# Kernel tuning notes

Hardware: AMD Instinct MI355X
Metric: run time of the kernel (lower is better)

## Reference

```python
import math
import jax, jax.numpy as jnp
import numpy as np

B, D, C = 2, 1024, 512          # (b*f with f=1), spatial tokens, channels
H, DH = 8, 64                   # heads, head dim (H*DH == C)
P = 32                          # past length == temporal_max_len
MAX_LEN = 32
HID = max(128, C // 2)          # refiner hidden

def make_pe():
    # sinusoidal APE buffer, shape [MAX_LEN, C]
    position = np.arange(MAX_LEN)[:, None].astype(np.float32)
    div_term = np.exp(np.arange(0, C, 2).astype(np.float32) * (-math.log(10000.0) / C))
    pe = np.zeros((MAX_LEN, C), dtype=np.float32)
    pe[:, 0::2] = np.sin(position * div_term)
    pe[:, 1::2] = np.cos(position * div_term)
    return jnp.asarray(pe)

def setup_inputs() -> dict:
    key = jax.random.key(0)
    ks = jax.random.split(key, 12)
    sc = 0.02
    return {
        "hidden_states": jax.random.normal(ks[0], (B, D, C), jnp.float32),
        "cached_hidden_states": jax.random.normal(ks[1], (B * D, P, C), jnp.float32),
        "Wq": jax.random.normal(ks[2], (C, C), jnp.float32) * sc,
        "Wk": jax.random.normal(ks[3], (C, C), jnp.float32) * sc,
        "Wv": jax.random.normal(ks[4], (C, C), jnp.float32) * sc,
        "Wo": jax.random.normal(ks[5], (C, C), jnp.float32) * sc,
        "bo": jnp.zeros((C,), jnp.float32),
        "W1": jax.random.normal(ks[6], (3 * C, HID), jnp.float32) * sc,
        "b1": jnp.zeros((HID,), jnp.float32),
        "W2": jax.random.normal(ks[7], (HID, 2 * C + 2), jnp.float32) * sc,
        "b2": jnp.zeros((2 * C + 2,), jnp.float32),
        "pe": make_pe(),
        "select_top_r": 8,
    }

def reference(hidden_states, cached_hidden_states, Wq, Wk, Wv, Wo, bo, W1, b1, W2, b2, pe, select_top_r):
    b, d, c = hidden_states.shape
    B0 = b * d
    # '(b f) d c -> (b d) f c' with f=1
    now = hidden_states.reshape(B0, 1, c)
    past = cached_hidden_states                      # [B0, P, C]
    # APE positional encoding
    now_pos = now + pe[:1][None]
    past_pos = past + pe[: past.shape[1]][None]
    # projections (no bias, diffusers CrossAttention style)
    q_now = now_pos @ Wq                             # [B0, 1, C]
    k_now = now_pos @ Wk
    v_now = now_pos @ Wv
    k_past = past_pos @ Wk                           # [B0, P, C]
    v_past = past_pos @ Wv
    # top-r key selection over past
    score = jnp.einsum('bqc,bpc->bqp', q_now, k_past)[:, 0]   # [B0, P]
    _, idx = jax.lax.top_k(score, select_top_r)               # [B0, R]
    k_sel = jnp.take_along_axis(k_past, idx[:, :, None], axis=1)  # [B0, R, C]
    v_sel = jnp.take_along_axis(v_past, idx[:, :, None], axis=1)
    # refiner MLP: concat(q, k, v) -> hidden -> 2C+2
    R = k_sel.shape[1]
    q_rep = jnp.broadcast_to(q_now, (B0, R, c))
    inp = jnp.concatenate([q_rep, k_sel, v_sel], axis=-1)     # [B0, R, 3C]
    h = jax.nn.gelu(inp @ W1 + b1, approximate=False)
    out = h @ W2 + b2                                         # [B0, R, 2C+2]
    dK, dV, log_s, logit_g = jnp.split(out, [c, 2 * c, 2 * c + 1], axis=-1)
    s = jax.nn.softplus(log_s) + 1e-5
    g = jax.nn.sigmoid(logit_g)
    k_sel = k_sel + g * dK * s
    v_sel = v_sel + g * dV * s
    # attention over [selected past ; now]
    key_ = jnp.concatenate([k_sel, k_now], axis=1)            # [B0, R+1, C]
    val_ = jnp.concatenate([v_sel, v_now], axis=1)
    L = key_.shape[1]
    qh = q_now.reshape(B0, 1, H, DH)
    kh = key_.reshape(B0, L, H, DH)
    vh = val_.reshape(B0, L, H, DH)
    scale = DH ** -0.5
    logits = jnp.einsum('bqhd,bkhd->bhqk', qh, kh) * scale
    attn = jax.nn.softmax(logits, axis=-1)
    ctx = jnp.einsum('bhqk,bkhd->bqhd', attn, vh).reshape(B0, 1, c)
    out_proj = ctx @ Wo + bo                                  # [B0, 1, C]
    # '(b d) f c -> (b f) d c' with f=1
    return out_proj.reshape(b, d, c)
```

## Files before the change

### kernel.cpp

```cpp
#include <hip/hip_runtime.h>
#include <math.h>


typedef __attribute__((ext_vector_type(8))) __bf16 bf16x8;
typedef __attribute__((ext_vector_type(4))) float f32x4;
typedef unsigned short u16;
typedef unsigned int u32;

static __device__ __forceinline__ float4 ld4(const float* p) { return *(const float4*)p; }
static __device__ __forceinline__ float gelu_exact(float x) {
  return 0.5f * x * (1.0f + erff(x * 0.70710678118654752f));
}
static __device__ __forceinline__ u16 f2bf(float f) {
  u32 u = __float_as_uint(f);
  u = (u + 0x7fffu + ((u >> 16) & 1u)) >> 16;
  return (u16)u;
}
static __device__ __forceinline__ float bf2f(u16 h) {
  return __uint_as_float(((u32)h) << 16);
}
static __device__ __forceinline__ u32 pk2(float a, float b) {
  return (u32)f2bf(a) | ((u32)f2bf(b) << 16);
}
static __device__ __forceinline__ void ld8bf(const u16* p, float* o) {
  int4 v = *(const int4*)p;
  o[0] = bf2f((u16)((u32)v.x & 0xffffu)); o[1] = bf2f((u16)(((u32)v.x) >> 16));
  o[2] = bf2f((u16)((u32)v.y & 0xffffu)); o[3] = bf2f((u16)(((u32)v.y) >> 16));
  o[4] = bf2f((u16)((u32)v.z & 0xffffu)); o[5] = bf2f((u16)(((u32)v.z) >> 16));
  o[6] = bf2f((u16)((u32)v.w & 0xffffu)); o[7] = bf2f((u16)(((u32)v.w) >> 16));
}
static __device__ __forceinline__ void gld16(const void* g, void* l) {
  __builtin_amdgcn_global_load_lds((const __attribute__((address_space(1))) void*)g,
                                   (__attribute__((address_space(3))) void*)l, 16, 0, 0);
}

__global__ __launch_bounds__(256) void prep_all(
    const float* __restrict__ Wq, const float* __restrict__ Wk,
    const float* __restrict__ Wv, const float* __restrict__ W1,
    const float* __restrict__ W2, const float* __restrict__ Wo,
    u16* __restrict__ Wqkvt, u16* __restrict__ W1t,
    u16* __restrict__ W2t, u16* __restrict__ Wot,
    float* __restrict__ Wqk) {
  const int b = blockIdx.x;
  if (b < 1664) {
    __shared__ float t[32][33];
    const float* S; u16* D; int lds_, Kd, nx, t0;
    if (b < 256)       { S = Wq; D = Wqkvt;              lds_ = 512;  Kd = 512;  nx = 16; t0 = 0; }
    else if (b < 512)  { S = Wk; D = Wqkvt + 512 * 512;  lds_ = 512;  Kd = 512;  nx = 16; t0 = 256; }
    else if (b < 768)  { S = Wv; D = Wqkvt + 1024 * 512; lds_ = 512;  Kd = 512;  nx = 16; t0 = 512; }
    else if (b < 1152) { S = W1; D = W1t;                lds_ = 256;  Kd = 1536; nx = 8;  t0 = 768; }
    else if (b < 1408) { S = W2; D = W2t;                lds_ = 1026; Kd = 256;  nx = 32; t0 = 1152; }
    else               { S = Wo; D = Wot;                lds_ = 512;  Kd = 512;  nx = 16; t0 = 1408; }
    const int tile = b - t0;
    const int n0 = (tile % nx) << 5, k0 = (tile / nx) << 5;
    const int tx = threadIdx.x & 31, ty8 = threadIdx.x >> 5;
    for (int yy = ty8; yy < 32; yy += 8)
      t[yy][tx] = S[(size_t)(k0 + yy) * lds_ + n0 + tx];
    __syncthreads();
    for (int yy = ty8; yy < 32; yy += 8)
      D[(size_t)(n0 + yy) * Kd + k0 + tx] = f2bf(t[tx][yy]);
  } else {
    __shared__ float Aq[32][36];
    __shared__ float Bk[32][36];
    const int tile = b - 1664;
    const int c0 = (tile >> 4) << 5, j0 = (tile & 15) << 5;
    const int tid = threadIdx.x;
    const int r = tid >> 3, ic = (tid & 7) << 2;
    const int ty = tid >> 4, tx = tid & 15;
    float a00 = 0.f, a01 = 0.f, a10 = 0.f, a11 = 0.f;
    for (int i0 = 0; i0 < 512; i0 += 32) {
      float4 a = ld4(Wq + (size_t)(c0 + r) * 512 + i0 + ic);
      float4 bb = ld4(Wk + (size_t)(j0 + r) * 512 + i0 + ic);
      Aq[r][ic] = a.x; Aq[r][ic + 1] = a.y; Aq[r][ic + 2] = a.z; Aq[r][ic + 3] = a.w;
      Bk[r][ic] = bb.x; Bk[r][ic + 1] = bb.y; Bk[r][ic + 2] = bb.z; Bk[r][ic + 3] = bb.w;
      __syncthreads();
#pragma unroll
      for (int i = 0; i < 32; ++i) {
        float x0 = Aq[ty * 2][i], x1 = Aq[ty * 2 + 1][i];
        float y0 = Bk[tx * 2][i], y1 = Bk[tx * 2 + 1][i];
        a00 += x0 * y0; a01 += x0 * y1; a10 += x1 * y0; a11 += x1 * y1;
      }
      __syncthreads();
    }
    Wqk[(size_t)(c0 + ty * 2) * 512 + j0 + tx * 2]         = a00;
    Wqk[(size_t)(c0 + ty * 2) * 512 + j0 + tx * 2 + 1]     = a01;
    Wqk[(size_t)(c0 + ty * 2 + 1) * 512 + j0 + tx * 2]     = a10;
    Wqk[(size_t)(c0 + ty * 2 + 1) * 512 + j0 + tx * 2 + 1] = a11;
  }
}

__global__ __launch_bounds__(256) void qk_gemm(const float* __restrict__ A,
                                               const float* __restrict__ B,
                                               float* __restrict__ C,
                                               const float* __restrict__ pe) {
  __shared__ float As[16][68];
  __shared__ float Bs[16][68];
  const int tid = threadIdx.x;
  const int rm = blockIdx.y << 6, cn = blockIdx.x << 6;
  const int tx = tid & 15, ty = tid >> 4;
  const int ar = tid >> 2, ak = (tid & 3) << 2;
  const int bk = tid >> 4, bn = (tid & 15) << 2;
  const float* Ap = A + (size_t)(rm + ar) * 512;
  float acc[4][4] = {};
  for (int kt = 0; kt < 32; ++kt) {
    const int k0 = (kt << 4) + ak;
    float4 x = ld4(Ap + k0);
    float4 p4 = ld4(pe + k0);
    As[ak + 0][ar] = x.x + p4.x; As[ak + 1][ar] = x.y + p4.y;
    As[ak + 2][ar] = x.z + p4.z; As[ak + 3][ar] = x.w + p4.w;
    *(float4*)&Bs[bk][bn] = ld4(B + (size_t)((kt << 4) + bk) * 512 + cn + bn);
    __syncthreads();
#pragma unroll
    for (int kk = 0; kk < 16; ++kk) {
      float4 a = *(const float4*)&As[kk][ty << 2];
      float4 b = *(const float4*)&Bs[kk][tx << 2];
      acc[0][0] += a.x * b.x; acc[0][1] += a.x * b.y; acc[0][2] += a.x * b.z; acc[0][3] += a.x * b.w;
      acc[1][0] += a.y * b.x; acc[1][1] += a.y * b.y; acc[1][2] += a.y * b.z; acc[1][3] += a.y * b.w;
      acc[2][0] += a.z * b.x; acc[2][1] += a.z * b.y; acc[2][2] += a.z * b.z; acc[2][3] += a.z * b.w;
      acc[3][0] += a.w * b.x; acc[3][1] += a.w * b.y; acc[3][2] += a.w * b.z; acc[3][3] += a.w * b.w;
    }
    __syncthreads();
  }
  const int row0 = rm + (ty << 2), col0 = cn + (tx << 2);
#pragma unroll
  for (int i = 0; i < 4; ++i)
    *(float4*)(C + (size_t)(row0 + i) * 512 + col0) =
        make_float4(acc[i][0], acc[i][1], acc[i][2], acc[i][3]);
}

__global__ __launch_bounds__(256) void score_topk_gather(
    const float* __restrict__ QK, const float* __restrict__ cached,
    const float* __restrict__ pe, const float* __restrict__ hidden,
    u16* __restrict__ xh, u16* __restrict__ gsel) {
  __shared__ float sc[32];
  __shared__ int ix[8];
  const int b0 = blockIdx.x;
  const int tid = threadIdx.x;
  const int w = tid >> 6, lane = tid & 63;
  const int off = lane << 3;
  const float* qk = QK + (size_t)b0 * 512;
  float4 q0 = ld4(qk + off);
  float4 q1 = ld4(qk + off + 4);
  for (int i = 0; i < 8; ++i) {
    const int p = (w << 3) + i;
    const float* cp = cached + ((size_t)b0 * 32 + p) * 512 + off;
    const float* pp = pe + (size_t)p * 512 + off;
    float4 c0 = ld4(cp), c1 = ld4(cp + 4);
    float4 e0 = ld4(pp), e1 = ld4(pp + 4);
    float s = (c0.x + e0.x) * q0.x + (c0.y + e0.y) * q0.y +
              (c0.z + e0.z) * q0.z + (c0.w + e0.w) * q0.w +
              (c1.x + e1.x) * q1.x + (c1.y + e1.y) * q1.y +
              (c1.z + e1.z) * q1.z + (c1.w + e1.w) * q1.w;
#pragma unroll
    for (int d = 32; d > 0; d >>= 1) s += __shfl_xor(s, d);
    if (lane == 0) sc[p] = s;
  }
  __syncthreads();
  if (tid == 0) {
    for (int r = 0; r < 8; ++r) {
      float best = -INFINITY; int bi = 0;
      for (int p = 0; p < 32; ++p) {
        float v = sc[p];
        if (v > best) { best = v; bi = p; }
      }
      ix[r] = bi;
      sc[bi] = -INFINITY;
    }
  }
  __syncthreads();
#pragma unroll
  for (int rr = 0; rr < 2; ++rr) {
    const int rsel = w + (rr << 2);
    const int p = ix[rsel];
    const float* cp = cached + ((size_t)b0 * 32 + p) * 512 + off;
    const float* pp = pe + (size_t)p * 512 + off;
    float4 c0 = ld4(cp), c1 = ld4(cp + 4);
    float4 e0 = ld4(pp), e1 = ld4(pp + 4);
    int4 o;
    o.x = pk2(c0.x + e0.x, c0.y + e0.y);
    o.y = pk2(c0.z + e0.z, c0.w + e0.w);
    o.z = pk2(c1.x + e1.x, c1.y + e1.y);
    o.w = pk2(c1.z + e1.z, c1.w + e1.w);
    *(int4*)(gsel + (size_t)(b0 * 8 + rsel) * 512 + off) = o;
  }
  if (w == 0) {
    const float* hp = hidden + (size_t)b0 * 512 + off;
    float4 a = ld4(hp), b = ld4(hp + 4);
    float4 p0 = ld4(pe + off), p1 = ld4(pe + off + 4);
    int4 o;
    o.x = pk2(a.x + p0.x, a.y + p0.y);
    o.y = pk2(a.z + p0.z, a.w + p0.w);
    o.z = pk2(b.x + p1.x, b.y + p1.y);
    o.w = pk2(b.z + p1.z, b.w + p1.w);
    *(int4*)(xh + (size_t)b0 * 512 + off) = o;
  }
}

__global__ __launch_bounds__(256) void bgemm_fused1(
    const u16* __restrict__ gsel, const u16* __restrict__ xh,
    const u16* __restrict__ Wqkvt, u16* __restrict__ kvh,
    u16* __restrict__ Yh) {
  __shared__ u16 As[4096];
  __shared__ u16 Bs[4096];
  const int tid = threadIdx.x, lane = tid & 63, w = tid >> 6;
  const int bid = blockIdx.x;
  const int srow = tid >> 2, skoff = (tid & 3) << 3;
  const u16 *a0, *b0; u16* C; int ldc, rm, cn;
  if (bid < 1024) {
    rm = (bid >> 3) << 7; cn = (bid & 7) << 7;
    a0 = gsel + (size_t)(rm + srow) * 512 + skoff;
    b0 = Wqkvt + (size_t)(512 + cn + srow) * 512 + skoff;
    C = kvh; ldc = 1024;
  } else {
    const int b2 = bid - 1024;
    rm = (b2 / 12) << 7; cn = (b2 % 12) << 7;
    a0 = xh + (size_t)(rm + srow) * 512 + skoff;
    b0 = Wqkvt + (size_t)(cn + srow) * 512 + skoff;
    C = Yh; ldc = 1536;
  }
  const u16* a1 = a0 + (size_t)64 * 512;
  const u16* b1 = b0 + (size_t)64 * 512;
  u16* aD0 = As + (w << 9); u16* aD1 = As + 2048 + (w << 9);
  u16* bD0 = Bs + (w << 9); u16* bD1 = Bs + 2048 + (w << 9);
  const int arb = ((((w >> 1) << 6) + (lane & 15)) << 5) + ((lane >> 4) << 3);
  const int brb = ((((w & 1) << 6) + (lane & 15)) << 5) + ((lane >> 4) << 3);
  f32x4 acc[4][4];
#pragma unroll
  for (int i = 0; i < 4; ++i)
#pragma unroll
    for (int j = 0; j < 4; ++j) acc[i][j] = (f32x4){0.f, 0.f, 0.f, 0.f};
  for (int kt = 0; kt < 16; ++kt) {
    const int ko = kt << 5;
    if (kt) __syncthreads();
    gld16(a0 + ko, aD0); gld16(a1 + ko, aD1);
    gld16(b0 + ko, bD0); gld16(b1 + ko, bD1);
    __syncthreads();
    bf16x8 av[4], bv[4];
#pragma unroll
    for (int i = 0; i < 4; ++i) av[i] = *(const bf16x8*)(As + arb + (i << 9));
#pragma unroll
    for (int j = 0; j < 4; ++j) bv[j] = *(const bf16x8*)(Bs + brb + (j << 9));
#pragma unroll
    for (int i = 0; i < 4; ++i)
#pragma unroll
      for (int j = 0; j < 4; ++j)
        acc[i][j] = __builtin_amdgcn_mfma_f32_16x16x32_bf16(av[i], bv[j], acc[i][j], 0, 0, 0);
  }
  const int row0 = rm + ((w >> 1) << 6) + ((lane >> 4) << 2);
  const int col0 = cn + ((w & 1) << 6) + (lane & 15);
#pragma unroll
  for (int j = 0; j < 4; ++j) {
    const int col = col0 + (j << 4);
#pragma unroll
    for (int i = 0; i < 4; ++i)
#pragma unroll
      for (int r = 0; r < 4; ++r)
        C[(size_t)(row0 + (i << 4) + r) * ldc + col] = f2bf(acc[i][j][r]);
  }
}

__global__ __launch_bounds__(256) void mlp1_sg(
    const u16* __restrict__ Yh, const u16* __restrict__ kvh,
    const u16* __restrict__ W1t, const float* __restrict__ b1,
    const float* __restrict__ W2, const float* __restrict__ b2,
    u16* __restrict__ hb, float* __restrict__ sgv) {
  __shared__ u16 As[2048];
  __shared__ u16 Bs[8192];
  __shared__ float wa[256], wb[256];
  const int tid = threadIdx.x, lane = tid & 63, w = tid >> 6;
  const int rm = blockIdx.x << 6;
  const int srow = tid >> 2, skoff = (tid & 3) << 3;
  wa[tid] = W2[(size_t)tid * 1026 + 1024];
  wb[tid] = W2[(size_t)tid * 1026 + 1025];
  const int m0 = rm + srow;
  const u16* aq = Yh + (size_t)(m0 >> 3) * 1536 + skoff;
  const u16* akv = kvh + (size_t)m0 * 1024 + skoff;
  const u16* bsrc = W1t + (size_t)srow * 1536 + skoff;
  u16* aD = As + (w << 9);
  u16* bD0 = Bs + (w << 9);
  u16* bD1 = Bs + 2048 + (w << 9);
  u16* bD2 = Bs + 4096 + (w << 9);
  u16* bD3 = Bs + 6144 + (w << 9);
  const int arb = ((lane & 15) << 5) + ((lane >> 4) << 3);
  const int brb = (((w << 6) + (lane & 15)) << 5) + ((lane >> 4) << 3);
  f32x4 acc[4][4];
#pragma unroll
  for (int i = 0; i < 4; ++i)
#pragma unroll
    for (int j = 0; j < 4; ++j) acc[i][j] = (f32x4){0.f, 0.f, 0.f, 0.f};
  for (int kt = 0; kt < 48; ++kt) {
    const int ko = kt << 5;
    if (kt) __syncthreads();
    if (kt < 16) gld16(aq + ko, aD);
    else         gld16(akv + ko - 512, aD);
    gld16(bsrc + ko, bD0);
    gld16(bsrc + (size_t)64 * 1536 + ko, bD1);
    gld16(bsrc + (size_t)128 * 1536 + ko, bD2);
    gld16(bsrc + (size_t)192 * 1536 + ko, bD3);
    __syncthreads();
    bf16x8 av[4], bv[4];
#pragma unroll
    for (int i = 0; i < 4; ++i) av[i] = *(const bf16x8*)(As + arb + (i << 9));
#pragma unroll
    for (int j = 0; j < 4; ++j) bv[j] = *(const bf16x8*)(Bs + brb + (j << 9));
#pragma unroll
    for (int i = 0; i < 4; ++i)
#pragma unroll
      for (int j = 0; j < 4; ++j)
        acc[i][j] = __builtin_amdgcn_mfma_f32_16x16x32_bf16(av[i], bv[j], acc[i][j], 0, 0, 0);
  }
  const int row0 = rm + ((lane >> 4) << 2);
  const int col0 = (w << 6) + (lane & 15);
#pragma unroll
  for (int j = 0; j < 4; ++j) {
    const int col = col0 + (j << 4);
    const float bc = b1[col];
#pragma unroll
    for (int i = 0; i < 4; ++i)
#pragma unroll
      for (int r = 0; r < 4; ++r)
        hb[(size_t)(row0 + (i << 4) + r) * 256 + col] = f2bf(gelu_exact(acc[i][j][r] + bc));
  }
  __syncthreads();
  const int row = tid >> 2, q = tid & 3;
  const int rr = rm + row;
  const u16* hp = hb + (size_t)rr * 256 + (q << 6);
  float pa = 0.f, pb = 0.f;
  for (int c = 0; c < 64; c += 8) {
    float h[8]; ld8bf(hp + c, h);
    const int cb = (q << 6) + c;
#pragma unroll
    for (int t = 0; t < 8; ++t) { pa += h[t] * wa[cb + t]; pb += h[t] * wb[cb + t]; }
  }
  pa += __shfl_xor(pa, 1); pa += __shfl_xor(pa, 2);
  pb += __shfl_xor(pb, 1); pb += __shfl_xor(pb, 2);
  if (q == 0) {
    const float t0 = pa + b2[1024];
    const float t1 = pb + b2[1025];
    const float s = (t0 > 0.f ? t0 + log1pf(expf(-t0)) : log1pf(expf(t0))) + 1e-5f;
    const float g = 1.f / (1.f + expf(-t1));
    sgv[2 * rr] = s; sgv[2 * rr + 1] = g;
  }
}

__global__ __launch_bounds__(256) void bgemm_delta(
    const u16* __restrict__ hb, const u16* __restrict__ W2t,
    u16* __restrict__ kvh, const float* __restrict__ b2,
    const float* __restrict__ sgv) {
  __shared__ u16 As[4096];
  __shared__ u16 Bs[4096];
  const int tid = threadIdx.x, lane = tid & 63, w = tid >> 6;
  const int rm = blockIdx.y << 7, cn = blockIdx.x << 7;
  const int srow = tid >> 2, skoff = (tid & 3) << 3;
  const u16* a0 = hb + (size_t)(rm + srow) * 256 + skoff;
  const u16* a1 = a0 + (size_t)64 * 256;
  const u16* b0 = W2t + (size_t)(cn + srow) * 256 + skoff;
  const u16* b1 = b0 + (size_t)64 * 256;
  u16* aD0 = As + (w << 9); u16* aD1 = As + 2048 + (w << 9);
  u16* bD0 = Bs + (w << 9); u16* bD1 = Bs + 2048 + (w << 9);
  const int arb = ((((w >> 1) << 6) + (lane & 15)) << 5) + ((lane >> 4) << 3);
  const int brb = ((((w & 1) << 6) + (lane & 15)) << 5) + ((lane >> 4) << 3);
  f32x4 acc[4][4];
#pragma unroll
  for (int i = 0; i < 4; ++i)
#pragma unroll
    for (int j = 0; j < 4; ++j) acc[i][j] = (f32x4){0.f, 0.f, 0.f, 0.f};
  for (int kt = 0; kt < 8; ++kt) {
    const int ko = kt << 5;
    if (kt) __syncthreads();
    gld16(a0 + ko, aD0); gld16(a1 + ko, aD1);
    gld16(b0 + ko, bD0); gld16(b1 + ko, bD1);
    __syncthreads();
    bf16x8 av[4], bv[4];
#pragma unroll
    for (int i = 0; i < 4; ++i) av[i] = *(const bf16x8*)(As + arb + (i << 9));
#pragma unroll
    for (int j = 0; j < 4; ++j) bv[j] = *(const bf16x8*)(Bs + brb + (j << 9));
#pragma unroll
    for (int i = 0; i < 4; ++i)
#pragma unroll
      for (int j = 0; j < 4; ++j)
        acc[i][j] = __builtin_amdgcn_mfma_f32_16x16x32_bf16(av[i], bv[j], acc[i][j], 0, 0, 0);
  }
  const int row0 = rm + ((w >> 1) << 6) + ((lane >> 4) << 2);
  const int col0 = cn + ((w & 1) << 6) + (lane & 15);
  float bc[4];
#pragma unroll
  for (int j = 0; j < 4; ++j) bc[j] = b2[col0 + (j << 4)];
#pragma unroll
  for (int i = 0; i < 4; ++i)
#pragma unroll
    for (int r = 0; r < 4; ++r) {
      const int rr = row0 + (i << 4) + r;
      const float gs = sgv[2 * rr] * sgv[2 * rr + 1];
      u16* p = kvh + (size_t)rr * 1024 + col0;
#pragma unroll
      for (int j = 0; j < 4; ++j) {
        const int o = j << 4;
        p[o] = f2bf(bf2f(p[o]) + gs * (acc[i][j][r] + bc[j]));
      }
    }
}

__global__ __launch_bounds__(256) void attn2(const u16* __restrict__ Yh,
                                             const u16* __restrict__ kvh,
                                             u16* __restrict__ ctxh) {
  const int w = threadIdx.x >> 6, lane = threadIdx.x & 63;
  const int b0 = (blockIdx.x << 2) + w;
  const int off = lane << 3;
  const u16* yr = Yh + (size_t)b0 * 1536;
  float qv[8]; ld8bf(yr + off, qv);
  float lg[9];
#pragma unroll
  for (int k = 0; k < 9; ++k) {
    const u16* kr = (k < 8) ? (kvh + (size_t)(b0 * 8 + k) * 1024 + off)
                            : (yr + 512 + off);
    float kv[8]; ld8bf(kr, kv);
    float s = qv[0] * kv[0] + qv[1] * kv[1] + qv[2] * kv[2] + qv[3] * kv[3] +
              qv[4] * kv[4] + qv[5] * kv[5] + qv[6] * kv[6] + qv[7] * kv[7];
    s += __shfl_xor(s, 1); s += __shfl_xor(s, 2); s += __shfl_xor(s, 4);
    lg[k] = s * 0.125f;
  }
  float m = lg[0];
#pragma unroll
  for (int k = 1; k < 9; ++k) m = fmaxf(m, lg[k]);
  float sum = 0.f;
#pragma unroll
  for (int k = 0; k < 9; ++k) { lg[k] = expf(lg[k] - m); sum += lg[k]; }
  const float inv = 1.f / sum;
  float c[8] = {0.f, 0.f, 0.f, 0.f, 0.f, 0.f, 0.f, 0.f};
#pragma unroll
  for (int k = 0; k < 9; ++k) {
    const u16* vr = (k < 8) ? (kvh + (size_t)(b0 * 8 + k) * 1024 + 512 + off)
                            : (yr + 1024 + off);
    float vv[8]; ld8bf(vr, vv);
    const float wk = lg[k] * inv;
#pragma unroll
    for (int t = 0; t < 8; ++t) c[t] += wk * vv[t];
  }
  int4 o;
  o.x = pk2(c[0], c[1]); o.y = pk2(c[2], c[3]);
  o.z = pk2(c[4], c[5]); o.w = pk2(c[6], c[7]);
  *(int4*)(ctxh + (size_t)b0 * 512 + off) = o;
}

__global__ __launch_bounds__(256) void bgemm_out(
    const u16* __restrict__ ctxh, const u16* __restrict__ Wot,
    float* __restrict__ out, const float* __restrict__ bo) {
  __shared__ u16 As[4096];
  __shared__ u16 Bs[4096];
  const int tid = threadIdx.x, lane = tid & 63, w = tid >> 6;
  const int rm = blockIdx.y << 7, cn = blockIdx.x << 7;
  const int srow = tid >> 2, skoff = (tid & 3) << 3;
  const u16* a0 = ctxh + (size_t)(rm + srow) * 512 + skoff;
  const u16* a1 = a0 + (size_t)64 * 512;
  const u16* b0 = Wot + (size_t)(cn + srow) * 512 + skoff;
  const u16* b1 = b0 + (size_t)64 * 512;
  u16* aD0 = As + (w << 9); u16* aD1 = As + 2048 + (w << 9);
  u16* bD0 = Bs + (w << 9); u16* bD1 = Bs + 2048 + (w << 9);
  const int arb = ((((w >> 1) << 6) + (lane & 15)) << 5) + ((lane >> 4) << 3);
  const int brb = ((((w & 1) << 6) + (lane & 15)) << 5) + ((lane >> 4) << 3);
  f32x4 acc[4][4];
#pragma unroll
  for (int i = 0; i < 4; ++i)
#pragma unroll
    for (int j = 0; j < 4; ++j) acc[i][j] = (f32x4){0.f, 0.f, 0.f, 0.f};
  for (int kt = 0; kt < 16; ++kt) {
    const int ko = kt << 5;
    if (kt) __syncthreads();
    gld16(a0 + ko, aD0); gld16(a1 + ko, aD1);
    gld16(b0 + ko, bD0); gld16(b1 + ko, bD1);
    __syncthreads();
    bf16x8 av[4], bv[4];
#pragma unroll
    for (int i = 0; i < 4; ++i) av[i] = *(const bf16x8*)(As + arb + (i << 9));
#pragma unroll
    for (int j = 0; j < 4; ++j) bv[j] = *(const bf16x8*)(Bs + brb + (j << 9));
#pragma unroll
    for (int i = 0; i < 4; ++i)
#pragma unroll
      for (int j = 0; j < 4; ++j)
        acc[i][j] = __builtin_amdgcn_mfma_f32_16x16x32_bf16(av[i], bv[j], acc[i][j], 0, 0, 0);
  }
  const int row0 = rm + ((w >> 1) << 6) + ((lane >> 4) << 2);
  const int col0 = cn + ((w & 1) << 6) + (lane & 15);
  float bc[4];
#pragma unroll
  for (int j = 0; j < 4; ++j) bc[j] = bo[col0 + (j << 4)];
#pragma unroll
  for (int j = 0; j < 4; ++j)
#pragma unroll
    for (int i = 0; i < 4; ++i)
#pragma unroll
      for (int r = 0; r < 4; ++r)
        out[(size_t)(row0 + (i << 4) + r) * 512 + col0 + (j << 4)] = acc[i][j][r] + bc[j];
}

extern "C" void kernel_launch(void* const* d_in, const int* in_sizes, int n_in,
                              void* d_out, int out_size, void* d_ws, size_t ws_size,
                              hipStream_t stream) {
  const float* hidden = (const float*)d_in[0];
  const float* cached = (const float*)d_in[1];
  const float* Wq = (const float*)d_in[2];
  const float* Wk = (const float*)d_in[3];
  const float* Wv = (const float*)d_in[4];
  const float* Wo = (const float*)d_in[5];
  const float* bo = (const float*)d_in[6];
  const float* W1 = (const float*)d_in[7];
  const float* b1 = (const float*)d_in[8];
  const float* W2 = (const float*)d_in[9];
  const float* b2 = (const float*)d_in[10];
  const float* pe = (const float*)d_in[11];

  float* ws = (float*)d_ws;
  float* Wqk = ws;
  float* qkb = Wqk + 262144;
  float* sgv = qkb + 1048576;
  u16* Wqkvt = (u16*)(sgv + 32768);
  u16* W1t   = Wqkvt + 786432;
  u16* W2t   = W1t + 393216;
  u16* Wot   = W2t + 262144;
  u16* xh    = Wot + 262144;
  u16* gsel  = xh + 1048576;
  u16* Yh    = gsel + 8388608;
  u16* kvh   = Yh + 3145728;
  u16* hb    = kvh + 16777216;
  u16* ctxh  = hb + 4194304;
  float* out = (float*)d_out;
  (void)in_sizes; (void)n_in; (void)out_size; (void)ws_size;

  prep_all<<<dim3(1920), 256, 0, stream>>>(Wq, Wk, Wv, W1, W2, Wo,
                                           Wqkvt, W1t, W2t, Wot, Wqk);
  qk_gemm<<<dim3(8, 32), 256, 0, stream>>>(hidden, Wqk, qkb, pe);
  score_topk_gather<<<dim3(2048), 256, 0, stream>>>(qkb, cached, pe, hidden, xh, gsel);
  bgemm_fused1<<<dim3(1216), 256, 0, stream>>>(gsel, xh, Wqkvt, kvh, Yh);
  mlp1_sg<<<dim3(256), 256, 0, stream>>>(Yh, kvh, W1t, b1, W2, b2, hb, sgv);
  bgemm_delta<<<dim3(8, 128), 256, 0, stream>>>(hb, W2t, kvh, b2, sgv);
  attn2<<<dim3(512), 256, 0, stream>>>(Yh, kvh, ctxh);
  bgemm_out<<<dim3(4, 16), 256, 0, stream>>>(ctxh, Wot, out, bo);
}
```

Measured before the change: 443.0 us.

## Double K-tile depth in MFMA GEMMs and swap operands for vectorized epilogue stores

All four bf16 MFMA GEMM kernels now stage a 64-wide K slice per iteration instead of 32. That halves the loop trip count and the number of barrier pairs, at the cost of doubling LDS per block. The MFMA operands are swapped so each lane holds four consecutive output columns. This lets the epilogues write packed int2 bf16 or float4 fp32 values and read bias as float4, replacing the earlier scalar, strided stores. The larger LDS footprint may lower occupancy.

```diff
diff --git a/kernel.cpp b/kernel.cpp
--- a/kernel.cpp
+++ b/kernel.cpp
@@ -32,6 +32,14 @@
 static __device__ __forceinline__ void gld16(const void* g, void* l) {
   __builtin_amdgcn_global_load_lds((const __attribute__((address_space(1))) void*)g,
                                    (__attribute__((address_space(3))) void*)l, 16, 0, 0);
+}
+template <int NI>
+static __device__ __forceinline__ void stageT(u16* __restrict__ lds,
+                                              const u16* __restrict__ sp,
+                                              int ldk, int w) {
+#pragma unroll
+  for (int i = 0; i < NI; ++i)
+    gld16(sp + (size_t)(i << 5) * ldk, lds + (w << 9) + (i << 11));
 }
 
 __global__ __launch_bounds__(256) void prep_all(
@@ -200,62 +208,61 @@
     const u16* __restrict__ gsel, const u16* __restrict__ xh,
     const u16* __restrict__ Wqkvt, u16* __restrict__ kvh,
     u16* __restrict__ Yh) {
-  __shared__ u16 As[4096];
-  __shared__ u16 Bs[4096];
+  __shared__ u16 As[8192];
+  __shared__ u16 Bs[8192];
   const int tid = threadIdx.x, lane = tid & 63, w = tid >> 6;
   const int bid = blockIdx.x;
-  const int srow = tid >> 2, skoff = (tid & 3) << 3;
-  const u16 *a0, *b0; u16* C; int ldc, rm, cn;
+  int rm, cn, ldc; const u16 *Ab, *Bb; u16* C;
   if (bid < 1024) {
     rm = (bid >> 3) << 7; cn = (bid & 7) << 7;
-    a0 = gsel + (size_t)(rm + srow) * 512 + skoff;
-    b0 = Wqkvt + (size_t)(512 + cn + srow) * 512 + skoff;
-    C = kvh; ldc = 1024;
+    Ab = gsel; Bb = Wqkvt + (size_t)512 * 512; C = kvh; ldc = 1024;
   } else {
     const int b2 = bid - 1024;
     rm = (b2 / 12) << 7; cn = (b2 % 12) << 7;
-    a0 = xh + (size_t)(rm + srow) * 512 + skoff;
-    b0 = Wqkvt + (size_t)(cn + srow) * 512 + skoff;
-    C = Yh; ldc = 1536;
-  }
-  const u16* a1 = a0 + (size_t)64 * 512;
-  const u16* b1 = b0 + (size_t)64 * 512;
-  u16* aD0 = As + (w << 9); u16* aD1 = As + 2048 + (w << 9);
-  u16* bD0 = Bs + (w << 9); u16* bD1 = Bs + 2048 + (w << 9);
-  const int arb = ((((w >> 1) << 6) + (lane & 15)) << 5) + ((lane >> 4) << 3);
-  const int brb = ((((w & 1) << 6) + (lane & 15)) << 5) + ((lane >> 4) << 3);
+    Ab = xh; Bb = Wqkvt; C = Yh; ldc = 1536;
+  }
+  const int lrow = (w << 3) + (lane >> 3), lko = (lane & 7) << 3;
+  const u16* ap = Ab + (size_t)(rm + lrow) * 512 + lko;
+  const u16* bp = Bb + (size_t)(cn + lrow) * 512 + lko;
+  const int aoff = ((w >> 1) << 12) + ((lane & 15) << 6) + ((lane >> 4) << 3);
+  const int boff = ((w & 1) << 12) + ((lane & 15) << 6) + ((lane >> 4) << 3);
   f32x4 acc[4][4];
 #pragma unroll
   for (int i = 0; i < 4; ++i)
 #pragma unroll
     for (int j = 0; j < 4; ++j) acc[i][j] = (f32x4){0.f, 0.f, 0.f, 0.f};
-  for (int kt = 0; kt < 16; ++kt) {
-    const int ko = kt << 5;
+  for (int kt = 0; kt < 8; ++kt) {
     if (kt) __syncthreads();
-    gld16(a0 + ko, aD0); gld16(a1 + ko, aD1);
-    gld16(b0 + ko, bD0); gld16(b1 + ko, bD1);
-    __syncthreads();
-    bf16x8 av[4], bv[4];
-#pragma unroll
-    for (int i = 0; i < 4; ++i) av[i] = *(const bf16x8*)(As + arb + (i << 9));
-#pragma unroll
-    for (int j = 0; j < 4; ++j) bv[j] = *(const bf16x8*)(Bs + brb + (j << 9));
-#pragma unroll
-    for (int i = 0; i < 4; ++i)
-#pragma unroll
-      for (int j = 0; j < 4; ++j)
-        acc[i][j] = __builtin_amdgcn_mfma_f32_16x16x32_bf16(av[i], bv[j], acc[i][j], 0, 0, 0);
-  }
-  const int row0 = rm + ((w >> 1) << 6) + ((lane >> 4) << 2);
-  const int col0 = cn + ((w & 1) << 6) + (lane & 15);
-#pragma unroll
-  for (int j = 0; j < 4; ++j) {
-    const int col = col0 + (j << 4);
-#pragma unroll
-    for (int i = 0; i < 4; ++i)
-#pragma unroll
-      for (int r = 0; r < 4; ++r)
-        C[(size_t)(row0 + (i << 4) + r) * ldc + col] = f2bf(acc[i][j][r]);
+    stageT<4>(As, ap, 512, w);
+    stageT<4>(Bs, bp, 512, w);
+    ap += 64; bp += 64;
+    __syncthreads();
+#pragma unroll
+    for (int s = 0; s < 2; ++s) {
+      bf16x8 av[4], bv[4];
+#pragma unroll
+      for (int i = 0; i < 4; ++i) av[i] = *(const bf16x8*)(As + aoff + (i << 10) + (s << 5));
+#pragma unroll
+      for (int j = 0; j < 4; ++j) bv[j] = *(const bf16x8*)(Bs + boff + (j << 10) + (s << 5));
+#pragma unroll
+      for (int i = 0; i < 4; ++i)
+#pragma unroll
+        for (int j = 0; j < 4; ++j)
+          acc[i][j] = __builtin_amdgcn_mfma_f32_16x16x32_bf16(bv[j], av[i], acc[i][j], 0, 0, 0);
+    }
+  }
+  const int row0 = rm + ((w >> 1) << 6) + (lane & 15);
+  const int col0 = cn + ((w & 1) << 6) + ((lane >> 4) << 2);
+#pragma unroll
+  for (int i = 0; i < 4; ++i) {
+    u16* cp = C + (size_t)(row0 + (i << 4)) * ldc + col0;
+#pragma unroll
+    for (int j = 0; j < 4; ++j) {
+      int2 o;
+      o.x = (int)pk2(acc[i][j][0], acc[i][j][1]);
+      o.y = (int)pk2(acc[i][j][2], acc[i][j][3]);
+      *(int2*)(cp + (j << 4)) = o;
+    }
   }
 }
 
@@ -264,62 +271,66 @@
     const u16* __restrict__ W1t, const float* __restrict__ b1,
     const float* __restrict__ W2, const float* __restrict__ b2,
     u16* __restrict__ hb, float* __restrict__ sgv) {
-  __shared__ u16 As[2048];
-  __shared__ u16 Bs[8192];
+  __shared__ u16 As[4096];
+  __shared__ u16 Bs[16384];
   __shared__ float wa[256], wb[256];
   const int tid = threadIdx.x, lane = tid & 63, w = tid >> 6;
   const int rm = blockIdx.x << 6;
-  const int srow = tid >> 2, skoff = (tid & 3) << 3;
   wa[tid] = W2[(size_t)tid * 1026 + 1024];
   wb[tid] = W2[(size_t)tid * 1026 + 1025];
-  const int m0 = rm + srow;
-  const u16* aq = Yh + (size_t)(m0 >> 3) * 1536 + skoff;
-  const u16* akv = kvh + (size_t)m0 * 1024 + skoff;
-  const u16* bsrc = W1t + (size_t)srow * 1536 + skoff;
-  u16* aD = As + (w << 9);
-  u16* bD0 = Bs + (w << 9);
-  u16* bD1 = Bs + 2048 + (w << 9);
-  u16* bD2 = Bs + 4096 + (w << 9);
-  u16* bD3 = Bs + 6144 + (w << 9);
-  const int arb = ((lane & 15) << 5) + ((lane >> 4) << 3);
-  const int brb = (((w << 6) + (lane & 15)) << 5) + ((lane >> 4) << 3);
+  const int lrow = (w << 3) + (lane >> 3), lko = (lane & 7) << 3;
+  const u16* aq0  = Yh + (size_t)((rm + lrow) >> 3) * 1536 + lko;
+  const u16* aq1  = Yh + (size_t)((rm + lrow + 32) >> 3) * 1536 + lko;
+  const u16* akv0 = kvh + (size_t)(rm + lrow) * 1024 + lko;
+  const u16* akv1 = kvh + (size_t)(rm + lrow + 32) * 1024 + lko;
+  const u16* bp = W1t + (size_t)lrow * 1536 + lko;
+  const int aoff = ((lane & 15) << 6) + ((lane >> 4) << 3);
+  const int boff = (w << 12) + aoff;
   f32x4 acc[4][4];
 #pragma unroll
   for (int i = 0; i < 4; ++i)
 #pragma unroll
     for (int j = 0; j < 4; ++j) acc[i][j] = (f32x4){0.f, 0.f, 0.f, 0.f};
-  for (int kt = 0; kt < 48; ++kt) {
-    const int ko = kt << 5;
+  for (int kt = 0; kt < 24; ++kt) {
+    const int ko = kt << 6;
     if (kt) __syncthreads();
-    if (kt < 16) gld16(aq + ko, aD);
-    else         gld16(akv + ko - 512, aD);
-    gld16(bsrc + ko, bD0);
-    gld16(bsrc + (size_t)64 * 1536 + ko, bD1);
-    gld16(bsrc + (size_t)128 * 1536 + ko, bD2);
-    gld16(bsrc + (size_t)192 * 1536 + ko, bD3);
-    __syncthreads();
-    bf16x8 av[4], bv[4];
-#pragma unroll
-    for (int i = 0; i < 4; ++i) av[i] = *(const bf16x8*)(As + arb + (i << 9));
-#pragma unroll
-    for (int j = 0; j < 4; ++j) bv[j] = *(const bf16x8*)(Bs + brb + (j << 9));
-#pragma unroll
-    for (int i = 0; i < 4; ++i)
-#pragma unroll
-      for (int j = 0; j < 4; ++j)
-        acc[i][j] = __builtin_amdgcn_mfma_f32_16x16x32_bf16(av[i], bv[j], acc[i][j], 0, 0, 0);
-  }
-  const int row0 = rm + ((lane >> 4) << 2);
-  const int col0 = (w << 6) + (lane & 15);
-#pragma unroll
-  for (int j = 0; j < 4; ++j) {
-    const int col = col0 + (j << 4);
-    const float bc = b1[col];
-#pragma unroll
-    for (int i = 0; i < 4; ++i)
-#pragma unroll
-      for (int r = 0; r < 4; ++r)
-        hb[(size_t)(row0 + (i << 4) + r) * 256 + col] = f2bf(gelu_exact(acc[i][j][r] + bc));
+    if (kt < 8) {
+      gld16(aq0 + ko, As + (w << 9));
+      gld16(aq1 + ko, As + (w << 9) + 2048);
+    } else {
+      gld16(akv0 + ko - 512, As + (w << 9));
+      gld16(akv1 + ko - 512, As + (w << 9) + 2048);
+    }
+    stageT<8>(Bs, bp, 1536, w);
+    bp += 64;
+    __syncthreads();
+#pragma unroll
+    for (int s = 0; s < 2; ++s) {
+      bf16x8 av[4], bv[4];
+#pragma unroll
+      for (int i = 0; i < 4; ++i) av[i] = *(const bf16x8*)(As + aoff + (i << 10) + (s << 5));
+#pragma unroll
+      for (int j = 0; j < 4; ++j) bv[j] = *(const bf16x8*)(Bs + boff + (j << 10) + (s << 5));
+#pragma unroll
+      for (int i = 0; i < 4; ++i)
+#pragma unroll
+        for (int j = 0; j < 4; ++j)
+          acc[i][j] = __builtin_amdgcn_mfma_f32_16x16x32_bf16(bv[j], av[i], acc[i][j], 0, 0, 0);
+    }
+  }
+  const int row0 = rm + (lane & 15);
+  const int col0 = (w << 6) + ((lane >> 4) << 2);
+#pragma unroll
+  for (int i = 0; i < 4; ++i) {
+    u16* hp = hb + (size_t)(row0 + (i << 4)) * 256 + col0;
+#pragma unroll
+    for (int j = 0; j < 4; ++j) {
+      float4 bb = ld4(b1 + col0 + (j << 4));
+      int2 o;
+      o.x = (int)pk2(gelu_exact(acc[i][j][0] + bb.x), gelu_exact(acc[i][j][1] + bb.y));
+      o.y = (int)pk2(gelu_exact(acc[i][j][2] + bb.z), gelu_exact(acc[i][j][3] + bb.w));
+      *(int2*)(hp + (j << 4)) = o;
+    }
   }
   __syncthreads();
   const int row = tid >> 2, q = tid & 3;
@@ -347,59 +358,62 @@
     const u16* __restrict__ hb, const u16* __restrict__ W2t,
     u16* __restrict__ kvh, const float* __restrict__ b2,
     const float* __restrict__ sgv) {
-  __shared__ u16 As[4096];
-  __shared__ u16 Bs[4096];
+  __shared__ u16 As[8192];
+  __shared__ u16 Bs[8192];
   const int tid = threadIdx.x, lane = tid & 63, w = tid >> 6;
   const int rm = blockIdx.y << 7, cn = blockIdx.x << 7;
-  const int srow = tid >> 2, skoff = (tid & 3) << 3;
-  const u16* a0 = hb + (size_t)(rm + srow) * 256 + skoff;
-  const u16* a1 = a0 + (size_t)64 * 256;
-  const u16* b0 = W2t + (size_t)(cn + srow) * 256 + skoff;
-  const u16* b1 = b0 + (size_t)64 * 256;
-  u16* aD0 = As + (w << 9); u16* aD1 = As + 2048 + (w << 9);
-  u16* bD0 = Bs + (w << 9); u16* bD1 = Bs + 2048 + (w << 9);
-  const int arb = ((((w >> 1) << 6) + (lane & 15)) << 5) + ((lane >> 4) << 3);
-  const int brb = ((((w & 1) << 6) + (lane & 15)) << 5) + ((lane >> 4) << 3);
+  const int lrow = (w << 3) + (lane >> 3), lko = (lane & 7) << 3;
+  const u16* ap = hb + (size_t)(rm + lrow) * 256 + lko;
+  const u16* bp = W2t + (size_t)(cn + lrow) * 256 + lko;
+  const int aoff = ((w >> 1) << 12) + ((lane & 15) << 6) + ((lane >> 4) << 3);
+  const int boff = ((w & 1) << 12) + ((lane & 15) << 6) + ((lane >> 4) << 3);
   f32x4 acc[4][4];
 #pragma unroll
   for (int i = 0; i < 4; ++i)
 #pragma unroll
     for (int j = 0; j < 4; ++j) acc[i][j] = (f32x4){0.f, 0.f, 0.f, 0.f};
-  for (int kt = 0; kt < 8; ++kt) {
-    const int ko = kt << 5;
+  for (int kt = 0; kt < 4; ++kt) {
     if (kt) __syncthreads();
-    gld16(a0 + ko, aD0); gld16(a1 + ko, aD1);
-    gld16(b0 + ko, bD0); gld16(b1 + ko, bD1);
-    __syncthreads();
-    bf16x8 av[4], bv[4];
-#pragma unroll
-    for (int i = 0; i < 4; ++i) av[i] = *(const bf16x8*)(As + arb + (i << 9));
-#pragma unroll
-    for (int j = 0; j < 4; ++j) bv[j] = *(const bf16x8*)(Bs + brb + (j << 9));
-#pragma unroll
-    for (int i = 0; i < 4; ++i)
-#pragma unroll
-      for (int j = 0; j < 4; ++j)
-        acc[i][j] = __builtin_amdgcn_mfma_f32_16x16x32_bf16(av[i], bv[j], acc[i][j], 0, 0, 0);
-  }
-  const int row0 = rm + ((w >> 1) << 6) + ((lane >> 4) << 2);
-  const int col0 = cn + ((w & 1) << 6) + (lane & 15);
-  float bc[4];
-#pragma unroll
-  for (int j = 0; j < 4; ++j) bc[j] = b2[col0 + (j << 4)];
-#pragma unroll
-  for (int i = 0; i < 4; ++i)
-#pragma unroll
-    for (int r = 0; r < 4; ++r) {
-      const int rr = row0 + (i << 4) + r;
-      const float gs = sgv[2 * rr] * sgv[2 * rr + 1];
-      u16* p = kvh + (size_t)rr * 1024 + col0;
-#pragma unroll
-      for (int j = 0; j < 4; ++j) {
-        const int o = j << 4;
-        p[o] = f2bf(bf2f(p[o]) + gs * (acc[i][j][r] + bc[j]));
-      }
-    }
+    stageT<4>(As, ap, 256, w);
+    stageT<4>(Bs, bp, 256, w);
+    ap += 64; bp += 64;
+    __syncthreads();
+#pragma unroll
+    for (int s = 0; s < 2; ++s) {
+      bf16x8 av[4], bv[4];
+#pragma unroll
+      for (int i = 0; i < 4; ++i) av[i] = *(const bf16x8*)(As + aoff + (i << 10) + (s << 5));
+#pragma unroll
+      for (int j = 0; j < 4; ++j) bv[j] = *(const bf16x8*)(Bs + boff + (j << 10) + (s << 5));
+#pragma unroll
+      for (int i = 0; i < 4; ++i)
+#pragma unroll
+        for (int j = 0; j < 4; ++j)
+          acc[i][j] = __builtin_amdgcn_mfma_f32_16x16x32_bf16(bv[j], av[i], acc[i][j], 0, 0, 0);
+    }
+  }
+  const int row0 = rm + ((w >> 1) << 6) + (lane & 15);
+  const int col0 = cn + ((w & 1) << 6) + ((lane >> 4) << 2);
+#pragma unroll
+  for (int i = 0; i < 4; ++i) {
+    const int row = row0 + (i << 4);
+    const float2 sg2 = *(const float2*)(sgv + (row << 1));
+    const float gs = sg2.x * sg2.y;
+    u16* cp = kvh + (size_t)row * 1024 + col0;
+#pragma unroll
+    for (int j = 0; j < 4; ++j) {
+      float4 bb = ld4(b2 + col0 + (j << 4));
+      int2 old = *(const int2*)(cp + (j << 4));
+      const float o0 = bf2f((u16)((u32)old.x & 0xffffu)) + gs * (acc[i][j][0] + bb.x);
+      const float o1 = bf2f((u16)(((u32)old.x) >> 16)) + gs * (acc[i][j][1] + bb.y);
+      const float o2 = bf2f((u16)((u32)old.y & 0xffffu)) + gs * (acc[i][j][2] + bb.z);
+      const float o3 = bf2f((u16)(((u32)old.y) >> 16)) + gs * (acc[i][j][3] + bb.w);
+      int2 nv;
+      nv.x = (int)pk2(o0, o1);
+      nv.y = (int)pk2(o2, o3);
+      *(int2*)(cp + (j << 4)) = nv;
+    }
+  }
 }
 
 __global__ __launch_bounds__(256) void attn2(const u16* __restrict__ Yh,
@@ -447,53 +461,52 @@
 __global__ __launch_bounds__(256) void bgemm_out(
     const u16* __restrict__ ctxh, const u16* __restrict__ Wot,
     float* __restrict__ out, const float* __restrict__ bo) {
-  __shared__ u16 As[4096];
-  __shared__ u16 Bs[4096];
+  __shared__ u16 As[8192];
+  __shared__ u16 Bs[8192];
   const int tid = threadIdx.x, lane = tid & 63, w = tid >> 6;
   const int rm = blockIdx.y << 7, cn = blockIdx.x << 7;
-  const int srow = tid >> 2, skoff = (tid & 3) << 3;
-  const u16* a0 = ctxh + (size_t)(rm + srow) * 512 + skoff;
-  const u16* a1 = a0 + (size_t)64 * 512;
-  const u16* b0 = Wot + (size_t)(cn + srow) * 512 + skoff;
-  const u16* b1 = b0 + (size_t)64 * 512;
-  u16* aD0 = As + (w << 9); u16* aD1 = As + 2048 + (w << 9);
-  u16* bD0 = Bs + (w << 9); u16* bD1 = Bs + 2048 + (w << 9);
-  const int arb = ((((w >> 1) << 6) + (lane & 15)) << 5) + ((lane >> 4) << 3);
-  const int brb = ((((w & 1) << 6) + (lane & 15)) << 5) + ((lane >> 4) << 3);
+  const int lrow = (w << 3) + (lane >> 3), lko = (lane & 7) << 3;
+  const u16* ap = ctxh + (size_t)(rm + lrow) * 512 + lko;
+  const u16* bp = Wot + (size_t)(cn + lrow) * 512 + lko;
+  const int aoff = ((w >> 1) << 12) + ((lane & 15) << 6) + ((lane >> 4) << 3);
+  const int boff = ((w & 1) << 12) + ((lane & 15) << 6) + ((lane >> 4) << 3);
   f32x4 acc[4][4];
 #pragma unroll
   for (int i = 0; i < 4; ++i)
 #pragma unroll
     for (int j = 0; j < 4; ++j) acc[i][j] = (f32x4){0.f, 0.f, 0.f, 0.f};
-  for (int kt = 0; kt < 16; ++kt) {
-    const int ko = kt << 5;
+  for (int kt = 0; kt < 8; ++kt) {
     if (kt) __syncthreads();
-    gld16(a0 + ko, aD0); gld16(a1 + ko, aD1);
-    gld16(b0 + ko, bD0); gld16(b1 + ko, bD1);
-    __syncthreads();
-    bf16x8 av[4], bv[4];
-#pragma unroll
-    for (int i = 0; i < 4; ++i) av[i] = *(const bf16x8*)(As + arb + (i << 9));
-#pragma unroll
-    for (int j = 0; j < 4; ++j) bv[j] = *(const bf16x8*)(Bs + brb + (j << 9));
-#pragma unroll
-    for (int i = 0; i < 4; ++i)
-#pragma unroll
-      for (int j = 0; j < 4; ++j)
-        acc[i][j] = __builtin_amdgcn_mfma_f32_16x16x32_bf16(av[i], bv[j], acc[i][j], 0, 0, 0);
-  }
-  const int row0 = rm + ((w >> 1) << 6) + ((lane >> 4) << 2);
-  const int col0 = cn + ((w & 1) << 6) + (lane & 15);
-  float bc[4];
-#pragma unroll
-  for (int j = 0; j < 4; ++j) bc[j] = bo[col0 + (j << 4)];
-#pragma unroll
-  for (int j = 0; j < 4; ++j)
-#pragma unroll
-    for (int i = 0; i < 4; ++i)
-#pragma unroll
-      for (int r = 0; r < 4; ++r)
-        out[(size_t)(row0 + (i << 4) + r) * 512 + col0 + (j << 4)] = acc[i][j][r] + bc[j];
+    stageT<4>(As, ap, 512, w);
+    stageT<4>(Bs, bp, 512, w);
+    ap += 64; bp += 64;
+    __syncthreads();
+#pragma unroll
+    for (int s = 0; s < 2; ++s) {
+      bf16x8 av[4], bv[4];
+#pragma unroll
+      for (int i = 0; i < 4; ++i) av[i] = *(const bf16x8*)(As + aoff + (i << 10) + (s << 5));
+#pragma unroll
+      for (int j = 0; j < 4; ++j) bv[j] = *(const bf16x8*)(Bs + boff + (j << 10) + (s << 5));
+#pragma unroll
+      for (int i = 0; i < 4; ++i)
+#pragma unroll
+        for (int j = 0; j < 4; ++j)
+          acc[i][j] = __builtin_amdgcn_mfma_f32_16x16x32_bf16(bv[j], av[i], acc[i][j], 0, 0, 0);
+    }
+  }
+  const int row0 = rm + ((w >> 1) << 6) + (lane & 15);
+  const int col0 = cn + ((w & 1) << 6) + ((lane >> 4) << 2);
+#pragma unroll
+  for (int i = 0; i < 4; ++i) {
+    float* op = out + (size_t)(row0 + (i << 4)) * 512 + col0;
+#pragma unroll
+    for (int j = 0; j < 4; ++j) {
+      float4 bb = ld4(bo + col0 + (j << 4));
+      *(float4*)(op + (j << 4)) = make_float4(acc[i][j][0] + bb.x, acc[i][j][1] + bb.y,
+                                              acc[i][j][2] + bb.z, acc[i][j][3] + bb.w);
+    }
+  }
 }
 
 extern "C" void kernel_launch(void* const* d_in, const int* in_sizes, int n_in,
```

Measured after the change: 452.9 us. 1.02x slower.
